# Kernel optimization log

Hardware: AMD Instinct MI355X
Metric: run time of the kernel (lower is better)

## Reference

```python
import jax, jax.numpy as jnp
import numpy as np

D_MODEL = 768
N_HEAD = 12
D_HEAD = 64


def setup_inputs() -> dict:
    key = jax.random.key(0)
    k1, k2, k3, k4, k5 = jax.random.split(key, 5)
    B, T = 8, 1024
    hidden_states = jax.random.normal(k1, (B, T, D_MODEL), dtype=jnp.float32)
    # torch Linear weights are [out, in]; we store [in, out] and use x @ W
    scale_attn = 1.0 / np.sqrt(D_MODEL)
    W_attn = jax.random.normal(k2, (D_MODEL, 3 * D_MODEL), dtype=jnp.float32) * scale_attn
    b_attn = jax.random.normal(k3, (3 * D_MODEL,), dtype=jnp.float32) * 0.02
    W_proj = jax.random.normal(k4, (D_MODEL, D_MODEL), dtype=jnp.float32) * scale_attn
    b_proj = jax.random.normal(k5, (D_MODEL,), dtype=jnp.float32) * 0.02
    return {"hidden_states": hidden_states, "W_attn": W_attn, "b_attn": b_attn,
            "W_proj": W_proj, "b_proj": b_proj}


def reference(hidden_states, W_attn, b_attn, W_proj, b_proj):
    B, T, _ = hidden_states.shape
    qkv = hidden_states @ W_attn + b_attn                     # [B, T, 3*D]
    Q, K, V = jnp.split(qkv, 3, axis=-1)
    def heads(x):  # [B, T, D] -> [B, H, T, d]
        return x.reshape(B, T, N_HEAD, D_HEAD).transpose(0, 2, 1, 3)
    Q, K, V = heads(Q), heads(K), heads(V)
    # past_key_values=None -> T_full == T, q_start == 0: standard causal mask
    scores = jnp.einsum('bhqd,bhkd->bhqk', Q, K) / np.sqrt(D_HEAD)
    causal = jnp.tril(jnp.ones((T, T), dtype=bool))
    scores = jnp.where(causal, scores, -jnp.inf)
    attn = jax.nn.softmax(scores, axis=-1)
    values = jnp.einsum('bhqk,bhkd->bhqd', attn, V)          # dropout = identity (eval)
    values = values.transpose(0, 2, 1, 3).reshape(B, T, D_MODEL)
    out = values @ W_proj + b_proj
    return out, K, V
```

## Files before the change

### kernel.cpp

```cpp
#include <hip/hip_runtime.h>
#include <stdint.h>

#define B_SZ 8
#define T_SZ 1024
#define DM   768
#define NH   12
#define DH   64
#define NTOK (B_SZ * T_SZ)
#define NOUT (NTOK * DM)
#define INF  __builtin_inff()

typedef unsigned short u16;
typedef __attribute__((ext_vector_type(8))) short short8;
typedef __attribute__((ext_vector_type(4))) short short4v;
typedef __attribute__((ext_vector_type(4))) float f32x4;

#define MFMA16x16x32 __builtin_amdgcn_mfma_f32_16x16x32_bf16

__device__ __forceinline__ u16 f2bf(float f) {
    unsigned u = __builtin_bit_cast(unsigned, f);
    u += 0x7fffu + ((u >> 16) & 1u);
    return (u16)(u >> 16);
}

__device__ __forceinline__ f32x4 max4(f32x4 a, f32x4 b) {
    f32x4 r; r.x = fmaxf(a.x, b.x); r.y = fmaxf(a.y, b.y);
    r.z = fmaxf(a.z, b.z); r.w = fmaxf(a.w, b.w); return r;
}
__device__ __forceinline__ f32x4 add4(f32x4 a, f32x4 b) {
    f32x4 r; r.x = a.x + b.x; r.y = a.y + b.y;
    r.z = a.z + b.z; r.w = a.w + b.w; return r;
}

__device__ __forceinline__ void gload16(const void* g, void* l) {
    __builtin_amdgcn_global_load_lds(
        (const __attribute__((address_space(1))) unsigned int*)(unsigned long long)(uintptr_t)g,
        (__attribute__((address_space(3))) unsigned int*)(unsigned int)(uintptr_t)l,
        16, 0, 0);
}

__global__ __launch_bounds__(256) void prep_kernel(
    const float* __restrict__ hs, u16* __restrict__ Xbf,
    const float* __restrict__ Wa, u16* __restrict__ WaT,
    const float* __restrict__ Wp, u16* __restrict__ WpT)
{
    __shared__ float tile[32][33];
    const int bid = blockIdx.x;
    if (bid < 6144) {
        const int i = bid * 1024 + threadIdx.x * 4;
        f32x4 v = *(const f32x4*)(hs + i);
        short4v o;
        o.x = (short)f2bf(v.x); o.y = (short)f2bf(v.y);
        o.z = (short)f2bf(v.z); o.w = (short)f2bf(v.w);
        *(short4v*)(Xbf + i) = o;
        return;
    }
    const float* in; u16* out; int R, C, bx, by;
    if (bid < 6144 + 1728) {
        const int lid = bid - 6144;
        in = Wa; out = WaT; R = 768; C = 2304; bx = lid % 72; by = lid / 72;
    } else {
        const int lid = bid - 7872;
        in = Wp; out = WpT; R = 768; C = 768; bx = lid % 24; by = lid / 24;
    }
    const int tx = threadIdx.x & 31, ty = threadIdx.x >> 5;
    const int c0 = bx * 32, r0 = by * 32;
    for (int i = ty; i < 32; i += 8)
        tile[i][tx] = in[(size_t)(r0 + i) * C + c0 + tx];
    __syncthreads();
    for (int i = ty; i < 32; i += 8)
        out[(size_t)(c0 + i) * R + r0 + tx] = f2bf(tile[tx][i]);
}

template <int EPI>
__global__ __launch_bounds__(256, 3) void gemm_k768_kernel(
    const u16* __restrict__ A, const u16* __restrict__ BT, const float* __restrict__ bias,
    u16* __restrict__ qbf, u16* __restrict__ kbf, u16* __restrict__ vtb,
    float* __restrict__ outK, float* __restrict__ outV, float* __restrict__ outP)
{
    __shared__ alignas(16) u16 SMEM[24576];
#define ASP(b) (SMEM + (b) * 4096)
#define BSP(b) (SMEM + 12288 + (b) * 4096)
    const int t   = threadIdx.x;
    const int wid = t >> 6, l = t & 63;
    const int lr  = l & 15, g = l >> 4;
    const int m0  = blockIdx.x * 128, n0 = blockIdx.y * 128;
    const int wm  = (wid >> 1) * 64, wn = (wid & 1) * 64;

    const int srow = t >> 2;
    const int sch  = ((t & 3) ^ ((srow >> 1) & 3)) * 8;
    const u16* ga0 = A  + (size_t)(m0 + srow) * 768 + sch;
    const u16* ga1 = A  + (size_t)(m0 + 64 + srow) * 768 + sch;
    const u16* gb0 = BT + (size_t)(n0 + srow) * 768 + sch;
    const u16* gb1 = BT + (size_t)(n0 + 64 + srow) * 768 + sch;

#define GSTAGE(buf, kt) do {                              \
        gload16(ga0 + (kt) * 32, ASP(buf) + t * 8);       \
        gload16(ga1 + (kt) * 32, ASP(buf) + 2048 + t * 8);\
        gload16(gb0 + (kt) * 32, BSP(buf) + t * 8);       \
        gload16(gb1 + (kt) * 32, BSP(buf) + 2048 + t * 8);\
    } while (0)

    const int fco = (g ^ ((lr >> 1) & 3)) * 8;

    f32x4 acc[4][4] = {};

#define COMPUTE(buf) do {                                                 \
        const u16* aB = ASP(buf);                                         \
        const u16* bB = BSP(buf);                                         \
        short8 af[4], bfr[4];                                             \
        _Pragma("unroll")                                                 \
        for (int i = 0; i < 4; ++i)                                       \
            af[i] = *(const short8*)(aB + (wm + i * 16 + lr) * 32 + fco); \
        _Pragma("unroll")                                                 \
        for (int j = 0; j < 4; ++j)                                       \
            bfr[j] = *(const short8*)(bB + (wn + j * 16 + lr) * 32 + fco);\
        __builtin_amdgcn_s_setprio(1);                                    \
        _Pragma("unroll")                                                 \
        for (int i = 0; i < 4; ++i)                                       \
            _Pragma("unroll")                                             \
            for (int j = 0; j < 4; ++j)                                   \
                acc[i][j] = MFMA16x16x32(af[i], bfr[j], acc[i][j], 0, 0, 0);\
        __builtin_amdgcn_s_setprio(0);                                    \
    } while (0)

#define WAITBAR(N) do {                                           \
        asm volatile("s_waitcnt vmcnt(" #N ")" ::: "memory");     \
        __builtin_amdgcn_s_barrier();                             \
        __builtin_amdgcn_sched_barrier(0);                        \
    } while (0)

    GSTAGE(0, 0); GSTAGE(1, 1);
    WAITBAR(4);

    #pragma unroll 1
    for (int i = 0; i < 7; ++i) {
        const int kt = i * 3;
        GSTAGE(2, kt + 2); COMPUTE(0); WAITBAR(4);
        GSTAGE(0, kt + 3); COMPUTE(1); WAITBAR(4);
        GSTAGE(1, kt + 4); COMPUTE(2); WAITBAR(4);
    }
    GSTAGE(2, 23); COMPUTE(0); WAITBAR(4);
    COMPUTE(1); WAITBAR(0);
    COMPUTE(2);
#undef GSTAGE
#undef COMPUTE
#undef WAITBAR

    if (EPI == 0) {
        __builtin_amdgcn_s_barrier();
        u16* EL = SMEM + wid * 4608;
        const int nbase = n0 + wn;
        const int which = nbase / 768;
        const int h = ((nbase - which * 768) >> 6);
        const int b = (m0 + wm) >> 10, tt0 = (m0 + wm) & 1023;
        const size_t rowbase = (size_t)(b * 12 + h) * 1024 + tt0;
        if (which == 0) {
            #pragma unroll
            for (int j = 0; j < 4; ++j) {
                const float bn = bias[nbase + j * 16 + lr];
                #pragma unroll
                for (int i = 0; i < 4; ++i)
                    #pragma unroll
                    for (int r = 0; r < 4; ++r) {
                        const int tau = i * 16 + g * 4 + r;
                        EL[tau * 72 + j * 16 + lr] =
                            f2bf((acc[i][j][r] + bn) * (0.125f * 1.44269504f));
                    }
            }
            asm volatile("s_waitcnt lgkmcnt(0)" ::: "memory");
            __builtin_amdgcn_sched_barrier(0);
            #pragma unroll
            for (int it = 0; it < 8; ++it) {
                const int q = it * 64 + l;
                const int tau = q >> 3, c = q & 7;
                *(short8*)(qbf + (rowbase + tau) * 64 + c * 8) =
                    *(const short8*)(EL + tau * 72 + c * 8);
            }
        } else if (which == 1) {
            #pragma unroll
            for (int j = 0; j < 4; ++j) {
                const float bn = bias[nbase + j * 16 + lr];
                #pragma unroll
                for (int i = 0; i < 4; ++i)
                    #pragma unroll
                    for (int r = 0; r < 4; ++r) {
                        const int tau = i * 16 + g * 4 + r;
                        const float v = acc[i][j][r] + bn;
                        EL[tau * 72 + j * 16 + lr] = f2bf(v);
                        outK[(rowbase + tau) * 64 + j * 16 + lr] = v;
                    }
            }
            asm volatile("s_waitcnt lgkmcnt(0)" ::: "memory");
            __builtin_amdgcn_sched_barrier(0);
            #pragma unroll
            for (int it = 0; it < 8; ++it) {
                const int q = it * 64 + l;
                const int tau = q >> 3, c = q & 7;
                *(short8*)(kbf + (rowbase + tau) * 64 + c * 8) =
                    *(const short8*)(EL + tau * 72 + c * 8);
            }
        } else {
            #pragma unroll
            for (int j = 0; j < 4; ++j) {
                const float bn = bias[nbase + j * 16 + lr];
                #pragma unroll
                for (int i = 0; i < 4; ++i)
                    #pragma unroll
                    for (int r = 0; r < 4; ++r) {
                        const int tau = i * 16 + g * 4 + r;
                        const float v = acc[i][j][r] + bn;
                        outV[(rowbase + tau) * 64 + j * 16 + lr] = v;
                        EL[(j * 16 + lr) * 72 + tau] = f2bf(v);
                    }
            }
            asm volatile("s_waitcnt lgkmcnt(0)" ::: "memory");
            __builtin_amdgcn_sched_barrier(0);
            u16* vt = vtb + (size_t)(b * 12 + h) * 65536 + tt0;
            #pragma unroll
            for (int it = 0; it < 8; ++it) {
                const int q = it * 64 + l;
                const int dd = q >> 3, c = q & 7;
                *(short8*)(vt + (size_t)dd * 1024 + c * 8) =
                    *(const short8*)(EL + dd * 72 + c * 8);
            }
        }
    } else {
        #pragma unroll
        for (int j = 0; j < 4; ++j) {
            const int n = n0 + wn + j * 16 + lr;
            const float bn = bias[n];
            #pragma unroll
            for (int i = 0; i < 4; ++i)
                #pragma unroll
                for (int r = 0; r < 4; ++r) {
                    const int m = m0 + wm + i * 16 + g * 4 + r;
                    outP[(size_t)m * 768 + n] = acc[i][j][r] + bn;
                }
        }
    }
#undef ASP
#undef BSP
}

__global__ __launch_bounds__(256, 3) void attn_kernel(
    const u16* __restrict__ Qb, const u16* __restrict__ Kb,
    const u16* __restrict__ Vt, u16* __restrict__ Ob)
{
    __shared__ alignas(16) u16 Ks[2][4096];
    __shared__ alignas(16) u16 Vs[2][4096];
    __shared__ alignas(16) u16 Pl[4][16 * 72];
    const int bh = blockIdx.x;
    const int t = threadIdx.x;
    const int wid = t >> 6, l = t & 63;
    const int c = l & 15, g = l >> 4;
    u16* P = Pl[wid];
    const u16* Kp = Kb + (size_t)bh * 65536;
    const u16* Vp = Vt + (size_t)bh * 65536;
    const int b = bh / 12, h = bh - (bh / 12) * 12;

    const int srow = t >> 3;
    const int sch  = (t & 7) ^ (srow & 7);
    const u16* Ksrc0 = Kp + (size_t)srow * 64 + sch * 8;
    const u16* Ksrc1 = Kp + (size_t)(srow + 32) * 64 + sch * 8;
    const u16* Vsrc0 = Vp + (size_t)srow * 1024 + sch * 8;
    const u16* Vsrc1 = Vp + (size_t)(srow + 32) * 1024 + sch * 8;

    const int fo0 = c * 64 + ((g ^ (c & 7)) * 8);
    const int fo1 = c * 64 + (((g + 4) ^ (c & 7)) * 8);

#define STAGE(buf, kt0) do {                                        \
        gload16(Ksrc0 + (size_t)(kt0) * 64, Ks[buf] + t * 8);       \
        gload16(Ksrc1 + (size_t)(kt0) * 64, Ks[buf] + 2048 + t * 8);\
        gload16(Vsrc0 + (kt0),              Vs[buf] + t * 8);       \
        gload16(Vsrc1 + (kt0),              Vs[buf] + 2048 + t * 8);\
    } while (0)

    #pragma unroll 1
    for (int pass = 0; pass < 2; ++pass) {
        const int tile = pass ? (15 - blockIdx.y) : blockIdx.y;
        const int qbase = tile * 64 + wid * 16;
        const int qg = qbase + c;
        const u16* Qp = Qb + ((size_t)bh * 1024 + qg) * 64 + g * 8;
        const short8 bq0 = *(const short8*)(Qp);
        const short8 bq1 = *(const short8*)(Qp + 32);

        f32x4 oacc[4] = {};
        float mrow = -INF, lpart = 0.f;
        const int nb = tile + 1;

        STAGE(0, 0);
        __syncthreads();
        int cur = 0;

        #pragma unroll 1
        for (int kb = 0; kb < nb; ++kb) {
            if (kb + 1 < nb) STAGE(cur ^ 1, (kb + 1) << 6);
            const u16* kB = Ks[cur];
            const u16* vB = Vs[cur];
            short8 af0[4], af1[4], vf0[4], vf1[4];
            #pragma unroll
            for (int j = 0; j < 4; ++j) {
                af0[j] = *(const short8*)(kB + j * 1024 + fo0);
                af1[j] = *(const short8*)(kB + j * 1024 + fo1);
            }
            #pragma unroll
            for (int dt = 0; dt < 4; ++dt) {
                vf0[dt] = *(const short8*)(vB + dt * 1024 + fo0);
                vf1[dt] = *(const short8*)(vB + dt * 1024 + fo1);
            }
            f32x4 s[4] = {};
            __builtin_amdgcn_s_setprio(1);
            #pragma unroll
            for (int j = 0; j < 4; ++j) {
                s[j] = MFMA16x16x32(af0[j], bq0, s[j], 0, 0, 0);
                s[j] = MFMA16x16x32(af1[j], bq1, s[j], 0, 0, 0);
            }
            __builtin_amdgcn_s_setprio(0);
            if (kb == nb - 1) {
                const int kt0 = kb << 6;
                #pragma unroll
                for (int j = 0; j < 4; ++j)
                    #pragma unroll
                    for (int r = 0; r < 4; ++r)
                        if (kt0 + j * 16 + g * 4 + r > qg) s[j][r] = -INF;
            }
            f32x4 mm = max4(max4(s[0], s[1]), max4(s[2], s[3]));
            float tm = fmaxf(fmaxf(mm.x, mm.y), fmaxf(mm.z, mm.w));
            tm = fmaxf(tm, __shfl_xor(tm, 16));
            tm = fmaxf(tm, __shfl_xor(tm, 32));
            const bool keep = (__all(tm <= mrow + 8.f) != 0);
            const float mnew = keep ? mrow : fmaxf(mrow, tm);
            if (!keep) {
                const float sc = exp2f(mrow - mnew);
                mrow = mnew;
                lpart *= sc;
                #pragma unroll
                for (int dt = 0; dt < 4; ++dt) {
                    oacc[dt][0] *= sc; oacc[dt][1] *= sc;
                    oacc[dt][2] *= sc; oacc[dt][3] *= sc;
                }
            }
            f32x4 p[4];
            #pragma unroll
            for (int j = 0; j < 4; ++j) {
                p[j].x = exp2f(s[j].x - mnew); p[j].y = exp2f(s[j].y - mnew);
                p[j].z = exp2f(s[j].z - mnew); p[j].w = exp2f(s[j].w - mnew);
            }
            f32x4 ps = add4(add4(p[0], p[1]), add4(p[2], p[3]));
            lpart += (ps.x + ps.y) + (ps.z + ps.w);
            #pragma unroll
            for (int j = 0; j < 4; ++j) {
                short4v w;
                w.x = (short)f2bf(p[j].x); w.y = (short)f2bf(p[j].y);
                w.z = (short)f2bf(p[j].z); w.w = (short)f2bf(p[j].w);
                *(short4v*)(P + c * 72 + j * 16 + g * 4) = w;
            }
            const short8 pf0 = *(const short8*)(P + c * 72 + g * 8);
            const short8 pf1 = *(const short8*)(P + c * 72 + 32 + g * 8);
            __builtin_amdgcn_s_setprio(1);
            #pragma unroll
            for (int dt = 0; dt < 4; ++dt) {
                oacc[dt] = MFMA16x16x32(vf0[dt], pf0, oacc[dt], 0, 0, 0);
                oacc[dt] = MFMA16x16x32(vf1[dt], pf1, oacc[dt], 0, 0, 0);
            }
            __builtin_amdgcn_s_setprio(0);
            __syncthreads();
            cur ^= 1;
        }
        float lsum = lpart;
        lsum += __shfl_xor(lsum, 16);
        lsum += __shfl_xor(lsum, 32);
        const float li = 1.f / lsum;
        #pragma unroll
        for (int dt = 0; dt < 4; ++dt) {
            short4v o;
            o.x = (short)f2bf(oacc[dt][0] * li);
            o.y = (short)f2bf(oacc[dt][1] * li);
            o.z = (short)f2bf(oacc[dt][2] * li);
            o.w = (short)f2bf(oacc[dt][3] * li);
            *(short4v*)(Ob + (size_t)(b * 1024 + qg) * 768 + h * 64 + dt * 16 + g * 4) = o;
        }
    }
#undef STAGE
}

extern "C" void kernel_launch(void* const* d_in, const int* in_sizes, int n_in,
                              void* d_out, int out_size, void* d_ws, size_t ws_size,
                              hipStream_t stream) {
    const float* hs = (const float*)d_in[0];
    const float* Wa = (const float*)d_in[1];
    const float* ba = (const float*)d_in[2];
    const float* Wp = (const float*)d_in[3];
    const float* bp = (const float*)d_in[4];
    float* out = (float*)d_out;

    u16* ws  = (u16*)d_ws;
    u16* Xbf = ws;
    u16* WaT = Xbf + NOUT;
    u16* WpT = WaT + 768 * 2304;
    u16* Qbf = WpT + 768 * 768;
    u16* Kbf = Qbf + NOUT;
    u16* VTb = Kbf + NOUT;
    u16* Obf = VTb + NOUT;

    prep_kernel<<<8448, 256, 0, stream>>>(hs, Xbf, Wa, WaT, Wp, WpT);
    gemm_k768_kernel<0><<<dim3(64, 18), 256, 0, stream>>>(
        Xbf, WaT, ba, Qbf, Kbf, VTb, out + NOUT, out + 2 * (size_t)NOUT, nullptr);
    attn_kernel<<<dim3(96, 8), 256, 0, stream>>>(Qbf, Kbf, VTb, Obf);
    gemm_k768_kernel<1><<<dim3(64, 6), 256, 0, stream>>>(
        Obf, WpT, bp, nullptr, nullptr, nullptr, nullptr, nullptr, out);
}
```

Measured before the change: 110.9 us.

## Add dedicated 64x128 projection GEMM and single-buffer V in attention

Replaces the generic 128-tile output projection GEMM with a dedicated kernel that uses 64x128 tiles, a three-stage LDS pipeline and explicit vmcnt waits. This doubles the block count along M so more of the machine is filled. The attention kernel now single-buffers V, loading it in the same iteration it is used and waiting on it just before the PV MFMAs. That frees LDS and registers so the kernel can raise launch bounds to 4 blocks per SM. The trade-off is that V load latency is less hidden, and each iteration gets an extra barrier.

```diff
diff --git a/kernel.cpp b/kernel.cpp
--- a/kernel.cpp
+++ b/kernel.cpp
@@ -243,12 +243,96 @@
 #undef BSP
 }
 
-__global__ __launch_bounds__(256, 3) void attn_kernel(
+__global__ __launch_bounds__(256, 4) void gemm_proj_kernel(
+    const u16* __restrict__ A, const u16* __restrict__ BT,
+    const float* __restrict__ bias, float* __restrict__ outP)
+{
+    __shared__ alignas(16) u16 As[3][64 * 32];
+    __shared__ alignas(16) u16 Bs[3][128 * 32];
+    const int t   = threadIdx.x;
+    const int wid = t >> 6, l = t & 63;
+    const int lr  = l & 15, g = l >> 4;
+    const int m0  = blockIdx.x * 64, n0 = blockIdx.y * 128;
+    const int wm  = (wid >> 1) * 32, wn = (wid & 1) * 64;
+
+    const int srow = t >> 2;
+    const int sch  = ((t & 3) ^ ((srow >> 1) & 3)) * 8;
+    const u16* ga0 = A  + (size_t)(m0 + srow) * 768 + sch;
+    const u16* gb0 = BT + (size_t)(n0 + srow) * 768 + sch;
+    const u16* gb1 = BT + (size_t)(n0 + 64 + srow) * 768 + sch;
+
+#define GSTAGE(buf, kt) do {                              \
+        gload16(ga0 + (kt) * 32, As[buf] + t * 8);        \
+        gload16(gb0 + (kt) * 32, Bs[buf] + t * 8);        \
+        gload16(gb1 + (kt) * 32, Bs[buf] + 2048 + t * 8); \
+    } while (0)
+
+    const int fco = (g ^ ((lr >> 1) & 3)) * 8;
+
+    f32x4 acc[2][4] = {};
+
+#define COMPUTE(buf) do {                                                 \
+        const u16* aB = As[buf];                                          \
+        const u16* bB = Bs[buf];                                          \
+        short8 af[2], bfr[4];                                             \
+        _Pragma("unroll")                                                 \
+        for (int i = 0; i < 2; ++i)                                       \
+            af[i] = *(const short8*)(aB + (wm + i * 16 + lr) * 32 + fco); \
+        _Pragma("unroll")                                                 \
+        for (int j = 0; j < 4; ++j)                                       \
+            bfr[j] = *(const short8*)(bB + (wn + j * 16 + lr) * 32 + fco);\
+        __builtin_amdgcn_s_setprio(1);                                    \
+        _Pragma("unroll")                                                 \
+        for (int i = 0; i < 2; ++i)                                       \
+            _Pragma("unroll")                                             \
+            for (int j = 0; j < 4; ++j)                                   \
+                acc[i][j] = MFMA16x16x32(af[i], bfr[j], acc[i][j], 0, 0, 0);\
+        __builtin_amdgcn_s_setprio(0);                                    \
+    } while (0)
+
+#define WAITBAR(N) do {                                           \
+        asm volatile("s_waitcnt vmcnt(" #N ")" ::: "memory");     \
+        __builtin_amdgcn_s_barrier();                             \
+        __builtin_amdgcn_sched_barrier(0);                        \
+    } while (0)
+
+    GSTAGE(0, 0); GSTAGE(1, 1);
+    WAITBAR(3);
+
+    #pragma unroll 1
+    for (int i = 0; i < 7; ++i) {
+        const int kt = i * 3;
+        GSTAGE(2, kt + 2); COMPUTE(0); WAITBAR(3);
+        GSTAGE(0, kt + 3); COMPUTE(1); WAITBAR(3);
+        GSTAGE(1, kt + 4); COMPUTE(2); WAITBAR(3);
+    }
+    GSTAGE(2, 23); COMPUTE(0); WAITBAR(3);
+    COMPUTE(1); WAITBAR(0);
+    COMPUTE(2);
+#undef GSTAGE
+#undef COMPUTE
+#undef WAITBAR
+
+    #pragma unroll
+    for (int j = 0; j < 4; ++j) {
+        const int n = n0 + wn + j * 16 + lr;
+        const float bn = bias[n];
+        #pragma unroll
+        for (int i = 0; i < 2; ++i)
+            #pragma unroll
+            for (int r = 0; r < 4; ++r) {
+                const int m = m0 + wm + i * 16 + g * 4 + r;
+                outP[(size_t)m * 768 + n] = acc[i][j][r] + bn;
+            }
+    }
+}
+
+__global__ __launch_bounds__(256, 4) void attn_kernel(
     const u16* __restrict__ Qb, const u16* __restrict__ Kb,
     const u16* __restrict__ Vt, u16* __restrict__ Ob)
 {
     __shared__ alignas(16) u16 Ks[2][4096];
-    __shared__ alignas(16) u16 Vs[2][4096];
+    __shared__ alignas(16) u16 Vs[4096];
     __shared__ alignas(16) u16 Pl[4][16 * 72];
     const int bh = blockIdx.x;
     const int t = threadIdx.x;
@@ -269,11 +353,13 @@
     const int fo0 = c * 64 + ((g ^ (c & 7)) * 8);
     const int fo1 = c * 64 + (((g + 4) ^ (c & 7)) * 8);
 
-#define STAGE(buf, kt0) do {                                        \
+#define STAGE_K(buf, kt0) do {                                      \
         gload16(Ksrc0 + (size_t)(kt0) * 64, Ks[buf] + t * 8);       \
         gload16(Ksrc1 + (size_t)(kt0) * 64, Ks[buf] + 2048 + t * 8);\
-        gload16(Vsrc0 + (kt0),              Vs[buf] + t * 8);       \
-        gload16(Vsrc1 + (kt0),              Vs[buf] + 2048 + t * 8);\
+    } while (0)
+#define STAGE_V(kt0) do {                                           \
+        gload16(Vsrc0 + (kt0), Vs + t * 8);                         \
+        gload16(Vsrc1 + (kt0), Vs + 2048 + t * 8);                  \
     } while (0)
 
     #pragma unroll 1
@@ -289,26 +375,22 @@
         float mrow = -INF, lpart = 0.f;
         const int nb = tile + 1;
 
-        STAGE(0, 0);
+        STAGE_K(0, 0);
         __syncthreads();
         int cur = 0;
 
         #pragma unroll 1
         for (int kb = 0; kb < nb; ++kb) {
-            if (kb + 1 < nb) STAGE(cur ^ 1, (kb + 1) << 6);
+            const int kt0 = kb << 6;
+            STAGE_V(kt0);
+            if (kb + 1 < nb) STAGE_K(cur ^ 1, kt0 + 64);
             const u16* kB = Ks[cur];
-            const u16* vB = Vs[cur];
-            short8 af0[4], af1[4], vf0[4], vf1[4];
+            short8 af0[4], af1[4];
             #pragma unroll
             for (int j = 0; j < 4; ++j) {
                 af0[j] = *(const short8*)(kB + j * 1024 + fo0);
                 af1[j] = *(const short8*)(kB + j * 1024 + fo1);
             }
-            #pragma unroll
-            for (int dt = 0; dt < 4; ++dt) {
-                vf0[dt] = *(const short8*)(vB + dt * 1024 + fo0);
-                vf1[dt] = *(const short8*)(vB + dt * 1024 + fo1);
-            }
             f32x4 s[4] = {};
             __builtin_amdgcn_s_setprio(1);
             #pragma unroll
@@ -318,7 +400,6 @@
             }
             __builtin_amdgcn_s_setprio(0);
             if (kb == nb - 1) {
-                const int kt0 = kb << 6;
                 #pragma unroll
                 for (int j = 0; j < 4; ++j)
                     #pragma unroll
@@ -356,8 +437,17 @@
                 w.z = (short)f2bf(p[j].z); w.w = (short)f2bf(p[j].w);
                 *(short4v*)(P + c * 72 + j * 16 + g * 4) = w;
             }
+            asm volatile("s_waitcnt vmcnt(0)" ::: "memory");
+            __builtin_amdgcn_s_barrier();
+            __builtin_amdgcn_sched_barrier(0);
             const short8 pf0 = *(const short8*)(P + c * 72 + g * 8);
             const short8 pf1 = *(const short8*)(P + c * 72 + 32 + g * 8);
+            short8 vf0[4], vf1[4];
+            #pragma unroll
+            for (int dt = 0; dt < 4; ++dt) {
+                vf0[dt] = *(const short8*)(Vs + dt * 1024 + fo0);
+                vf1[dt] = *(const short8*)(Vs + dt * 1024 + fo1);
+            }
             __builtin_amdgcn_s_setprio(1);
             #pragma unroll
             for (int dt = 0; dt < 4; ++dt) {
@@ -382,7 +472,8 @@
             *(short4v*)(Ob + (size_t)(b * 1024 + qg) * 768 + h * 64 + dt * 16 + g * 4) = o;
         }
     }
-#undef STAGE
+#undef STAGE_K
+#undef STAGE_V
 }
 
 extern "C" void kernel_launch(void* const* d_in, const int* in_sizes, int n_in,
@@ -408,6 +499,5 @@
     gemm_k768_kernel<0><<<dim3(64, 18), 256, 0, stream>>>(
         Xbf, WaT, ba, Qbf, Kbf, VTb, out + NOUT, out + 2 * (size_t)NOUT, nullptr);
     attn_kernel<<<dim3(96, 8), 256, 0, stream>>>(Qbf, Kbf, VTb, Obf);
-    gemm_k768_kernel<1><<<dim3(64, 6), 256, 0, stream>>>(
-        Obf, WpT, bp, nullptr, nullptr, nullptr, nullptr, nullptr, out);
-}
+    gemm_proj_kernel<<<dim3(128, 6), 256, 0, stream>>>(Obf, WpT, bp, out);
+}
```

Result: no change. 112.9 us (+1.8%).
